# Performance work log

Measured on AMD Instinct MI355X. Metric: run time of the kernel, lower is better.

Reference implementation:

```python
import jax, jax.numpy as jnp
from jax import lax
import numpy as np

B, H, W = 64, 256, 256          # batch, image height/width
CH = 16                          # channel (first conv out)
NCLS = 8                         # len(ansmap) + 1
HID = 128                        # LSTM hidden
ARR = 256                        # arr_size (flattened conv output = LSTM seq len)


def setup_inputs() -> dict:
    key = jax.random.key(0)
    ks = jax.random.split(key, 24)
    n = lambda k, s: jax.random.normal(k, s, dtype=jnp.float32)
    inp = {
        "x": n(ks[0], (B, 3, H, W)),
        # conv stage 1: Conv2d(3, CH, 2, 2) + BatchNorm2d(CH) (eval-mode stats)
        "conv1_w": n(ks[1], (CH, 3, 2, 2)) * 0.2,
        "conv1_b": n(ks[2], (CH,)) * 0.1,
        "bn1_g": jnp.ones((CH,), jnp.float32),
        "bn1_b": jnp.zeros((CH,), jnp.float32),
        "bn1_m": n(ks[3], (CH,)) * 0.1,
        "bn1_v": jax.random.uniform(ks[4], (CH,), jnp.float32, 0.5, 1.5),
        # conv stage 2: Conv2d(CH, 1, 2, 2) + BatchNorm2d(1)
        "conv2_w": n(ks[5], (1, CH, 2, 2)) * 0.2,
        "conv2_b": n(ks[6], (1,)) * 0.1,
        "bn2_g": jnp.ones((1,), jnp.float32),
        "bn2_b": jnp.zeros((1,), jnp.float32),
        "bn2_m": n(ks[7], (1,)) * 0.1,
        "bn2_v": jax.random.uniform(ks[8], (1,), jnp.float32, 0.5, 1.5),
        # prestack MLP: Linear(256,32) -> ReLU -> Linear(32,32) -> ReLU -> Linear(32,8) -> Softmax
        "pre_w1": n(ks[9], (32, ARR)) * 0.05,
        "pre_b1": n(ks[10], (32,)) * 0.05,
        "pre_w2": n(ks[11], (32, 32)) * 0.1,
        "pre_b2": n(ks[12], (32,)) * 0.05,
        "pre_w3": n(ks[13], (NCLS, 32)) * 0.1,
        "pre_b3": n(ks[14], (NCLS,)) * 0.05,
        # per-class LSTMs: LSTM(1, HID, batch_first=True), torch gate order i,f,g,o
        "lstm_wih": n(ks[15], (NCLS, 4 * HID, 1)) * 0.1,
        "lstm_whh": n(ks[16], (NCLS, 4 * HID, HID)) * 0.05,
        "lstm_bih": n(ks[17], (NCLS, 4 * HID)) * 0.05,
        "lstm_bhh": n(ks[18], (NCLS, 4 * HID)) * 0.05,
        # per-class persistent hidden state parameters hn[i]: (1, B, HID)
        "hn": n(ks[19], (NCLS, 1, B, HID)) * 0.1,
        # final stack: Linear(256, 8) after AvgPool2d((NCLS,1)) + Flatten
        "out_w": n(ks[20], (NCLS, ARR)) * 0.05,
        "out_b": n(ks[21], (NCLS,)) * 0.05,
    }
    return inp


def reference(x, conv1_w, conv1_b, bn1_g, bn1_b, bn1_m, bn1_v,
              conv2_w, conv2_b, bn2_g, bn2_b, bn2_m, bn2_v,
              pre_w1, pre_b1, pre_w2, pre_b2, pre_w3, pre_b3,
              lstm_wih, lstm_whh, lstm_bih, lstm_bhh, hn, out_w, out_b):
    def conv(z, w, b, s):
        y = lax.conv_general_dilated(z, w, (s, s), 'VALID',
                                     dimension_numbers=('NCHW', 'OIHW', 'NCHW'))
        return y + b[None, :, None, None]

    def bn(z, g, b, m, v):
        scale = g / jnp.sqrt(v + 1e-5)
        return (z - m[None, :, None, None]) * scale[None, :, None, None] + b[None, :, None, None]

    def maxpool2(z):
        return lax.reduce_window(z, -jnp.inf, lax.max, (1, 1, 2, 2), (1, 1, 2, 2), 'VALID')

    # conv feature extractor (the python map over x is just the batch dim)
    c = maxpool2(jax.nn.relu(bn(conv(x, conv1_w, conv1_b, 2), bn1_g, bn1_b, bn1_m, bn1_v)))
    c = maxpool2(jax.nn.relu(bn(conv(c, conv2_w, conv2_b, 2), bn2_g, bn2_b, bn2_m, bn2_v)))
    c = c.reshape(B, ARR)  # Flatten(0) per sample -> [B, 256]

    # prestack MLP + softmax over classes, then torch-style reshape (NCLS, B, 1)
    h1 = jax.nn.relu(c @ pre_w1.T + pre_b1)
    h2 = jax.nn.relu(h1 @ pre_w2.T + pre_b2)
    pre = jax.nn.softmax(h2 @ pre_w3.T + pre_b3, axis=1)  # [B, NCLS]
    pre = pre.reshape(NCLS, B, 1)  # row-major reshape, as in torch .reshape

    seq = c.reshape(B, ARR, 1)  # LSTM input, shared across all classes

    def lstm_last_unit(wih, whh, bih, bhh, h0):
        # wih [4H,1], whh [4H,H], h0 [B,H]; returns o[:, :, -1] -> [B, T]
        xg = jnp.einsum('bti,gi->btg', seq, wih) + bih  # precomputed input gates [B,T,4H]

        def step(carry, xgt):
            h, cc = carry
            gates = xgt + h @ whh.T + bhh  # [B, 4H]
            i, f, g, o = jnp.split(gates, 4, axis=-1)
            cc = jax.nn.sigmoid(f) * cc + jax.nn.sigmoid(i) * jnp.tanh(g)
            h = jax.nn.sigmoid(o) * jnp.tanh(cc)
            return (h, cc), h[:, -1]  # only last hidden feature is consumed

        (_, _), last = lax.scan(step, (h0, jnp.zeros_like(h0)), jnp.swapaxes(xg, 0, 1))
        return jnp.swapaxes(last, 0, 1)  # [B, T]

    h0 = hn[:, 0]  # [NCLS, B, HID]
    o_last = jax.vmap(lstm_last_unit)(lstm_wih, lstm_whh, lstm_bih, lstm_bhh, h0)  # [NCLS,B,T]

    r = (o_last * pre).transpose(1, 0, 2)  # [B, NCLS, T]
    avg = r.mean(axis=1)                   # AvgPool2d((NCLS,1)) + Flatten -> [B, T]
    return avg @ out_w.T + out_b           # [B, NCLS]
```

## Files before the change

kernel.cpp:

```cpp
#include <hip/hip_runtime.h>
#include <hip/hip_bf16.h>
#include <hip/hip_fp16.h>


typedef _Float16 h2_t __attribute__((ext_vector_type(2)));
typedef unsigned int u32x4 __attribute__((ext_vector_type(4)));

__device__ __forceinline__ float dot2f(unsigned int w, unsigned int h, float acc) {
    return __builtin_amdgcn_fdot2(__builtin_bit_cast(h2_t, w),
                                  __builtin_bit_cast(h2_t, h), acc, false);
}
__device__ __forceinline__ float sigmoidf_(float x) {
    return 1.0f / (1.0f + __expf(-x));
}
__device__ __forceinline__ float tanhf_(float x) {
    float t = __expf(-2.0f * fabsf(x));
    float r = (1.0f - t) / (1.0f + t);
    return copysignf(r, x);
}
__device__ __forceinline__ unsigned short f2h(float x) {
    __half h = __float2half(x);
    return *(unsigned short*)&h;
}

__global__ __launch_bounds__(256) void k_cvt(
    const float* __restrict__ w, unsigned int* __restrict__ wh)
{
    int i = blockIdx.x * 256 + threadIdx.x;
    float2 f = ((const float2*)w)[i];
    unsigned short lo = f2h(f.x), hi = f2h(f.y);
    wh[i] = ((unsigned int)hi << 16) | lo;
}

__global__ __launch_bounds__(256) void k_conv1(
    const float* __restrict__ x, const float* __restrict__ w,
    const float* __restrict__ cb, const float* __restrict__ g,
    const float* __restrict__ bb, const float* __restrict__ m,
    const float* __restrict__ v, float* __restrict__ c1)
{
    __shared__ __align__(16) float w1s[192];
    __shared__ float As[16], Cs[16];
    int tid = threadIdx.x;
    if (tid < 192) w1s[tid] = w[tid];
    if (tid < 16) {
        float s = g[tid] / sqrtf(v[tid] + 1e-5f);
        As[tid] = s;
        Cs[tid] = (cb[tid] - m[tid]) * s + bb[tid];
    }
    __syncthreads();

    int gid = blockIdx.x * 256 + tid;
    int b   = gid >> 12;
    int rem = gid & 4095;
    int oi  = rem >> 6, oj = rem & 63;

    float xr[3][4][4];
    #pragma unroll
    for (int ci = 0; ci < 3; ++ci) {
        #pragma unroll
        for (int r = 0; r < 4; ++r) {
            const float4 t4 = *(const float4*)(x +
                (((size_t)(b * 3 + ci) * 256 + (4 * oi + r)) * 256 + 4 * oj));
            xr[ci][r][0] = t4.x; xr[ci][r][1] = t4.y;
            xr[ci][r][2] = t4.z; xr[ci][r][3] = t4.w;
        }
    }
    const float4* w4 = (const float4*)w1s;
    #pragma unroll
    for (int co = 0; co < 16; ++co) {
        float val[2][2] = {{0.f, 0.f}, {0.f, 0.f}};
        #pragma unroll
        for (int ci = 0; ci < 3; ++ci) {
            float4 wq = w4[co * 3 + ci];
            #pragma unroll
            for (int pi = 0; pi < 2; ++pi) {
                #pragma unroll
                for (int pj = 0; pj < 2; ++pj) {
                    float a = val[pi][pj];
                    a = fmaf(xr[ci][2*pi  ][2*pj  ], wq.x, a);
                    a = fmaf(xr[ci][2*pi  ][2*pj+1], wq.y, a);
                    a = fmaf(xr[ci][2*pi+1][2*pj  ], wq.z, a);
                    a = fmaf(xr[ci][2*pi+1][2*pj+1], wq.w, a);
                    val[pi][pj] = a;
                }
            }
        }
        float A = As[co], C = Cs[co];
        float mx = 0.0f;
        #pragma unroll
        for (int pi = 0; pi < 2; ++pi)
            #pragma unroll
            for (int pj = 0; pj < 2; ++pj)
                mx = fmaxf(mx, fmaf(A, val[pi][pj], C));
        c1[((size_t)(b * 16 + co) * 64 + oi) * 64 + oj] = mx;
    }
}

__global__ __launch_bounds__(256) void k_conv2(
    const float* __restrict__ c1, const float* __restrict__ w2,
    const float* __restrict__ cb, const float* __restrict__ g,
    const float* __restrict__ bb, const float* __restrict__ m,
    const float* __restrict__ v, float* __restrict__ c)
{
    __shared__ float w2s[64];
    int tid = threadIdx.x;
    if (tid < 64) w2s[tid] = w2[tid];
    __syncthreads();
    float A2 = g[0] / sqrtf(v[0] + 1e-5f);
    float C2 = (cb[0] - m[0]) * A2 + bb[0];

    int gid = blockIdx.x * 256 + tid;
    int b   = gid >> 8;
    int rem = gid & 255;
    int oi  = rem >> 4, oj = rem & 15;

    float val[2][2] = {{0.f, 0.f}, {0.f, 0.f}};
    for (int ci = 0; ci < 16; ++ci) {
        float xr[4][4];
        #pragma unroll
        for (int r = 0; r < 4; ++r) {
            float4 t4 = *(const float4*)(c1 +
                (((size_t)(b * 16 + ci) * 64 + (4 * oi + r)) * 64 + 4 * oj));
            xr[r][0] = t4.x; xr[r][1] = t4.y; xr[r][2] = t4.z; xr[r][3] = t4.w;
        }
        float w0 = w2s[ci*4+0], w1 = w2s[ci*4+1], w2v = w2s[ci*4+2], w3 = w2s[ci*4+3];
        #pragma unroll
        for (int pi = 0; pi < 2; ++pi) {
            #pragma unroll
            for (int pj = 0; pj < 2; ++pj) {
                float a = val[pi][pj];
                a = fmaf(xr[2*pi  ][2*pj  ], w0, a);
                a = fmaf(xr[2*pi  ][2*pj+1], w1, a);
                a = fmaf(xr[2*pi+1][2*pj  ], w2v, a);
                a = fmaf(xr[2*pi+1][2*pj+1], w3, a);
                val[pi][pj] = a;
            }
        }
    }
    float mx = 0.0f;
    #pragma unroll
    for (int pi = 0; pi < 2; ++pi)
        #pragma unroll
        for (int pj = 0; pj < 2; ++pj)
            mx = fmaxf(mx, fmaf(A2, val[pi][pj], C2));
    c[(size_t)b * 256 + oi * 16 + oj] = mx;
}

__global__ __launch_bounds__(64) void k_mlp(
    const float* __restrict__ c,
    const float* __restrict__ w1, const float* __restrict__ b1,
    const float* __restrict__ w2, const float* __restrict__ b2,
    const float* __restrict__ w3, const float* __restrict__ b3,
    float* __restrict__ S)
{
    __shared__ __align__(16) float cs[256];
    __shared__ float h1s[32], h2s[32], ls[8];
    int b = blockIdx.x, tid = threadIdx.x;
    *(float4*)&cs[tid * 4] = *(const float4*)(c + (size_t)b * 256 + tid * 4);
    __syncthreads();
    if (tid < 32) {
        float acc = b1[tid];
        for (int k = 0; k < 256; ++k) acc = fmaf(cs[k], w1[tid * 256 + k], acc);
        h1s[tid] = fmaxf(acc, 0.f);
    }
    __syncthreads();
    if (tid < 32) {
        float acc = b2[tid];
        #pragma unroll
        for (int k = 0; k < 32; ++k) acc = fmaf(h1s[k], w2[tid * 32 + k], acc);
        h2s[tid] = fmaxf(acc, 0.f);
    }
    __syncthreads();
    if (tid < 8) {
        float acc = b3[tid];
        #pragma unroll
        for (int k = 0; k < 32; ++k) acc = fmaf(h2s[k], w3[tid * 32 + k], acc);
        ls[tid] = acc;
    }
    __syncthreads();
    if (tid == 0) {
        float mx = ls[0];
        #pragma unroll
        for (int k = 1; k < 8; ++k) mx = fmaxf(mx, ls[k]);
        float e[8]; float sum = 0.f;
        #pragma unroll
        for (int k = 0; k < 8; ++k) { e[k] = expf(ls[k] - mx); sum += e[k]; }
        float inv = 1.0f / sum;
        #pragma unroll
        for (int k = 0; k < 8; ++k) S[b * 8 + k] = e[k] * inv;
    }
}

__global__
__attribute__((amdgpu_flat_work_group_size(1024, 1024), amdgpu_waves_per_eu(4, 4)))
void k_lstm(
    const unsigned int* __restrict__ whh_h, const float* __restrict__ wih,
    const float* __restrict__ bih, const float* __restrict__ bhh,
    const float* __restrict__ hn,  const float* __restrict__ c,
    float* __restrict__ lasth)
{
    __shared__ __align__(16) unsigned short h_h[2][136];
    __shared__ float g_lds[2][512];
    __shared__ __align__(16) float c_lds[2][256];

    int tid   = threadIdx.x;
    int g     = tid >> 1;
    int kh    = tid & 1;
    int kcls  = blockIdx.x >> 5;
    int bbase = (blockIdx.x & 31) * 2;

    const u32x4* wp = (const u32x4*)(whh_h + ((size_t)(kcls * 512 + g)) * 64 + kh * 32);
    u32x4 u0 = wp[0], u1 = wp[1], u2 = wp[2], u3 = wp[3];
    u32x4 u4 = wp[4], u5 = wp[5], u6 = wp[6], u7 = wp[7];
    asm volatile("" : "+v"(u0), "+v"(u1), "+v"(u2), "+v"(u3),
                      "+v"(u4), "+v"(u5), "+v"(u6), "+v"(u7));

    float xw   = wih[kcls * 512 + g];
    float bias = bih[kcls * 512 + g] + bhh[kcls * 512 + g];
    int gtype  = g >> 7;

    if (tid < 256) {
        int b = tid >> 7, j = tid & 127;
        int js = j + ((j >> 6) << 3);
        h_h[b][js] = f2h(hn[((size_t)kcls * 64 + bbase + b) * 128 + j]);
    }
    if (tid < 128) {
        int f = tid * 4; int b = f >> 8; int off = f & 255;
        *(float4*)&c_lds[b][off] = *(const float4*)(c + (size_t)(bbase + b) * 256 + off);
    }
    float cc = 0.0f;
    __syncthreads();

    const u32x4* hq0 = (const u32x4*)((const unsigned int*)&h_h[0][0] + kh * 36);
    const u32x4* hq1 = (const u32x4*)((const unsigned int*)&h_h[1][0] + kh * 36);

#define DSTEP(I, A0, A1, B0, B1)                                        \
    {                                                                   \
        u32x4 q0 = hq0[I]; u32x4 q1 = hq1[I];                           \
        A0 = dot2f(u##I[0], q0[0], A0); A1 = dot2f(u##I[0], q1[0], A1); \
        B0 = dot2f(u##I[1], q0[1], B0); B1 = dot2f(u##I[1], q1[1], B1); \
        A0 = dot2f(u##I[2], q0[2], A0); A1 = dot2f(u##I[2], q1[2], A1); \
        B0 = dot2f(u##I[3], q0[3], B0); B1 = dot2f(u##I[3], q1[3], B1); \
    }

    for (int t = 0; t < 256; ++t) {
        float a0 = kh ? 0.0f : fmaf(c_lds[0][t], xw, bias);
        float a1 = kh ? 0.0f : fmaf(c_lds[1][t], xw, bias);
        float b0 = 0.0f, b1 = 0.0f;
        DSTEP(0, a0, a1, b0, b1) DSTEP(1, a0, a1, b0, b1)
        DSTEP(2, a0, a1, b0, b1) DSTEP(3, a0, a1, b0, b1)
        DSTEP(4, a0, a1, b0, b1) DSTEP(5, a0, a1, b0, b1)
        DSTEP(6, a0, a1, b0, b1) DSTEP(7, a0, a1, b0, b1)
        a0 += b0; a1 += b1;
        a0 += __shfl_xor(a0, 1);
        a1 += __shfl_xor(a1, 1);
        float vv = kh ? a1 : a0;
        vv = (gtype == 2) ? tanhf_(vv) : sigmoidf_(vv);
        g_lds[kh][g] = vv;
        __syncthreads();

        if (tid < 256) {
            int b = tid >> 7, j = tid & 127;
            float gi = g_lds[b][j];
            float gf = g_lds[b][128 + j];
            float gg = g_lds[b][256 + j];
            float go = g_lds[b][384 + j];
            cc = gf * cc + gi * gg;
            float h = go * tanhf_(cc);
            int js = j + ((j >> 6) << 3);
            h_h[b][js] = f2h(h);
            if (j == 127)
                lasth[((size_t)kcls * 64 + bbase + b) * 256 + t] = h;
        }
        __syncthreads();
    }
#undef DSTEP
}

__global__ __launch_bounds__(256) void k_out(
    const float* __restrict__ lasth, const float* __restrict__ S,
    const float* __restrict__ out_w, const float* __restrict__ out_b,
    float* __restrict__ out)
{
    __shared__ __align__(16) float avg[256];
    int b = blockIdx.x, t = threadIdx.x;
    float a = 0.f;
    #pragma unroll
    for (int k = 0; k < 8; ++k) {
        a = fmaf(S[k * 64 + b], lasth[((size_t)k * 64 + b) * 256 + t], a);
    }
    avg[t] = a * 0.125f;
    __syncthreads();
    if (t < 8) {
        float acc = out_b[t];
        for (int tt = 0; tt < 256; ++tt)
            acc = fmaf(avg[tt], out_w[t * 256 + tt], acc);
        out[b * 8 + t] = acc;
    }
}

extern "C" void kernel_launch(void* const* d_in, const int* in_sizes, int n_in,
                              void* d_out, int out_size, void* d_ws, size_t ws_size,
                              hipStream_t stream) {
    const float* x       = (const float*)d_in[0];
    const float* conv1_w = (const float*)d_in[1];
    const float* conv1_b = (const float*)d_in[2];
    const float* bn1_g   = (const float*)d_in[3];
    const float* bn1_b   = (const float*)d_in[4];
    const float* bn1_m   = (const float*)d_in[5];
    const float* bn1_v   = (const float*)d_in[6];
    const float* conv2_w = (const float*)d_in[7];
    const float* conv2_b = (const float*)d_in[8];
    const float* bn2_g   = (const float*)d_in[9];
    const float* bn2_b   = (const float*)d_in[10];
    const float* bn2_m   = (const float*)d_in[11];
    const float* bn2_v   = (const float*)d_in[12];
    const float* pre_w1  = (const float*)d_in[13];
    const float* pre_b1  = (const float*)d_in[14];
    const float* pre_w2  = (const float*)d_in[15];
    const float* pre_b2  = (const float*)d_in[16];
    const float* pre_w3  = (const float*)d_in[17];
    const float* pre_b3  = (const float*)d_in[18];
    const float* lstm_wih = (const float*)d_in[19];
    const float* lstm_whh = (const float*)d_in[20];
    const float* lstm_bih = (const float*)d_in[21];
    const float* lstm_bhh = (const float*)d_in[22];
    const float* hn      = (const float*)d_in[23];
    const float* out_w   = (const float*)d_in[24];
    const float* out_b   = (const float*)d_in[25];

    float* ws    = (float*)d_ws;
    float* c1    = ws;
    float* c     = c1 + 4194304;
    float* S     = c + 16384;
    float* lasth = S + 512;
    unsigned int* whh_h = (unsigned int*)c1;

    k_conv1<<<1024, 256, 0, stream>>>(x, conv1_w, conv1_b, bn1_g, bn1_b, bn1_m, bn1_v, c1);
    k_conv2<<<64, 256, 0, stream>>>(c1, conv2_w, conv2_b, bn2_g, bn2_b, bn2_m, bn2_v, c);
    k_mlp<<<64, 64, 0, stream>>>(c, pre_w1, pre_b1, pre_w2, pre_b2, pre_w3, pre_b3, S);
    k_cvt<<<1024, 256, 0, stream>>>(lstm_whh, whh_h);
    k_lstm<<<256, 1024, 0, stream>>>(whh_h, lstm_wih, lstm_bih, lstm_bhh, hn, c, lasth);
    k_out<<<64, 256, 0, stream>>>(lasth, S, out_w, out_b, (float*)d_out);
}
```

Measured before the change: 319.5 us.

## Broadcast hidden state via readlane and move LSTM K-split across waves

Each wave now owns 64 gates for one K-half, so the two halves of a gate are in different waves. Each lane loads one packed half2 of h from LDS, and the values are broadcast with v_readlane into scalar registers for the fdot2 operations. This replaces the per-lane 128-bit LDS vector reads and the shuffle reduction. Partial sums go through a larger LDS buffer, and the nonlinearities move into the 256-thread cell-update phase, which adds readlane instructions and serialises more activation work there.

```diff
diff --git a/kernel.cpp b/kernel.cpp
--- a/kernel.cpp
+++ b/kernel.cpp
@@ -199,13 +199,15 @@
     const float* __restrict__ hn,  const float* __restrict__ c,
     float* __restrict__ lasth)
 {
-    __shared__ __align__(16) unsigned short h_h[2][136];
-    __shared__ float g_lds[2][512];
+    __shared__ __align__(4) unsigned short h_s[2][128];
+    __shared__ float g_part[2][2][512];
     __shared__ __align__(16) float c_lds[2][256];
 
     int tid   = threadIdx.x;
-    int g     = tid >> 1;
-    int kh    = tid & 1;
+    int lane  = tid & 63;
+    int w     = tid >> 6;
+    int kh    = w & 1;
+    int g     = ((w >> 1) << 6) | lane;
     int kcls  = blockIdx.x >> 5;
     int bbase = (blockIdx.x & 31) * 2;
 
@@ -217,12 +219,10 @@
 
     float xw   = wih[kcls * 512 + g];
     float bias = bih[kcls * 512 + g] + bhh[kcls * 512 + g];
-    int gtype  = g >> 7;
 
     if (tid < 256) {
         int b = tid >> 7, j = tid & 127;
-        int js = j + ((j >> 6) << 3);
-        h_h[b][js] = f2h(hn[((size_t)kcls * 64 + bbase + b) * 128 + j]);
+        h_s[b][j] = f2h(hn[((size_t)kcls * 64 + bbase + b) * 128 + j]);
     }
     if (tid < 128) {
         int f = tid * 4; int b = f >> 8; int off = f & 255;
@@ -231,50 +231,48 @@
     float cc = 0.0f;
     __syncthreads();
 
-    const u32x4* hq0 = (const u32x4*)((const unsigned int*)&h_h[0][0] + kh * 36);
-    const u32x4* hq1 = (const u32x4*)((const unsigned int*)&h_h[1][0] + kh * 36);
-
-#define DSTEP(I, A0, A1, B0, B1)                                        \
-    {                                                                   \
-        u32x4 q0 = hq0[I]; u32x4 q1 = hq1[I];                           \
-        A0 = dot2f(u##I[0], q0[0], A0); A1 = dot2f(u##I[0], q1[0], A1); \
-        B0 = dot2f(u##I[1], q0[1], B0); B1 = dot2f(u##I[1], q1[1], B1); \
-        A0 = dot2f(u##I[2], q0[2], A0); A1 = dot2f(u##I[2], q1[2], A1); \
-        B0 = dot2f(u##I[3], q0[3], B0); B1 = dot2f(u##I[3], q1[3], B1); \
+    const unsigned int* hp0 = (const unsigned int*)&h_s[0][0];
+    const unsigned int* hp1 = (const unsigned int*)&h_s[1][0];
+    int hidx = kh * 32 + (lane & 31);
+
+#define DQ(Q)                                                              \
+    {                                                                      \
+        unsigned int s_;                                                   \
+        s_ = __builtin_amdgcn_readlane(hr0, 4*(Q)+0); a0 = dot2f(u##Q[0], s_, a0); \
+        s_ = __builtin_amdgcn_readlane(hr1, 4*(Q)+0); a1 = dot2f(u##Q[0], s_, a1); \
+        s_ = __builtin_amdgcn_readlane(hr0, 4*(Q)+1); a0 = dot2f(u##Q[1], s_, a0); \
+        s_ = __builtin_amdgcn_readlane(hr1, 4*(Q)+1); a1 = dot2f(u##Q[1], s_, a1); \
+        s_ = __builtin_amdgcn_readlane(hr0, 4*(Q)+2); a0 = dot2f(u##Q[2], s_, a0); \
+        s_ = __builtin_amdgcn_readlane(hr1, 4*(Q)+2); a1 = dot2f(u##Q[2], s_, a1); \
+        s_ = __builtin_amdgcn_readlane(hr0, 4*(Q)+3); a0 = dot2f(u##Q[3], s_, a0); \
+        s_ = __builtin_amdgcn_readlane(hr1, 4*(Q)+3); a1 = dot2f(u##Q[3], s_, a1); \
     }
 
     for (int t = 0; t < 256; ++t) {
+        unsigned int hr0 = hp0[hidx];
+        unsigned int hr1 = hp1[hidx];
         float a0 = kh ? 0.0f : fmaf(c_lds[0][t], xw, bias);
         float a1 = kh ? 0.0f : fmaf(c_lds[1][t], xw, bias);
-        float b0 = 0.0f, b1 = 0.0f;
-        DSTEP(0, a0, a1, b0, b1) DSTEP(1, a0, a1, b0, b1)
-        DSTEP(2, a0, a1, b0, b1) DSTEP(3, a0, a1, b0, b1)
-        DSTEP(4, a0, a1, b0, b1) DSTEP(5, a0, a1, b0, b1)
-        DSTEP(6, a0, a1, b0, b1) DSTEP(7, a0, a1, b0, b1)
-        a0 += b0; a1 += b1;
-        a0 += __shfl_xor(a0, 1);
-        a1 += __shfl_xor(a1, 1);
-        float vv = kh ? a1 : a0;
-        vv = (gtype == 2) ? tanhf_(vv) : sigmoidf_(vv);
-        g_lds[kh][g] = vv;
+        DQ(0) DQ(1) DQ(2) DQ(3) DQ(4) DQ(5) DQ(6) DQ(7)
+        g_part[kh][0][g] = a0;
+        g_part[kh][1][g] = a1;
         __syncthreads();
 
         if (tid < 256) {
             int b = tid >> 7, j = tid & 127;
-            float gi = g_lds[b][j];
-            float gf = g_lds[b][128 + j];
-            float gg = g_lds[b][256 + j];
-            float go = g_lds[b][384 + j];
+            float gi = sigmoidf_(g_part[0][b][j]       + g_part[1][b][j]);
+            float gf = sigmoidf_(g_part[0][b][128 + j] + g_part[1][b][128 + j]);
+            float gg = tanhf_  (g_part[0][b][256 + j] + g_part[1][b][256 + j]);
+            float go = sigmoidf_(g_part[0][b][384 + j] + g_part[1][b][384 + j]);
             cc = gf * cc + gi * gg;
             float h = go * tanhf_(cc);
-            int js = j + ((j >> 6) << 3);
-            h_h[b][js] = f2h(h);
+            h_s[b][j] = f2h(h);
             if (j == 127)
                 lasth[((size_t)kcls * 64 + bbase + b) * 256 + t] = h;
         }
         __syncthreads();
     }
-#undef DSTEP
+#undef DQ
 }
 
 __global__ __launch_bounds__(256) void k_out(
```

New measurement: 383.9 us. 1.2x slower.
